# Optimization experiments

Measured on AMD Instinct MI355X. Metric: run time of the kernel, lower is better.

## Reference

```python
import jax, jax.numpy as jnp
import numpy as np

CONF = 0.25
IOU = 0.7
MAX_DET = 300
IMG_H = 1280
IMG_W = 1280
KPT_SHAPE = (17, 3)
MAX_NMS = 3000
BS = 16
N_ANCH = 33600  # (1280/8)^2 + (1280/16)^2 + (1280/32)^2


def setup_inputs() -> dict:
    key = jax.random.key(0)
    k1, k2, k3, k4 = jax.random.split(key, 4)
    # realistic YOLO head outputs: centers in image, positive w/h, conf in (0,1)
    cxy = jax.random.uniform(k1, (BS, 2, N_ANCH)) * jnp.array([IMG_W, IMG_H], jnp.float32).reshape(1, 2, 1)
    wh = jax.random.uniform(k2, (BS, 2, N_ANCH)) * 200.0 + 4.0
    conf = jax.random.uniform(k3, (BS, 1, N_ANCH))
    kpts = jax.random.uniform(k4, (BS, 51, N_ANCH)) * float(IMG_W)
    preds = jnp.concatenate([cxy, wh, conf, kpts], axis=1).astype(jnp.float32)
    return {"preds": preds}


def _pairwise_iou(boxes):
    # boxes: [M, 4] xyxy
    area = (boxes[:, 2] - boxes[:, 0]) * (boxes[:, 3] - boxes[:, 1])
    lt = jnp.maximum(boxes[:, None, :2], boxes[None, :, :2])
    rb = jnp.minimum(boxes[:, None, 2:], boxes[None, :, 2:])
    wh = jnp.clip(rb - lt, 0.0)
    inter = wh[..., 0] * wh[..., 1]
    return inter / (area[:, None] + area[None, :] - inter + 1e-9)


def _nms_keep(boxes, valid):
    # greedy NMS over score-descending boxes; returns bool keep mask [M]
    M = boxes.shape[0]
    idx = jnp.arange(M)
    supp = (_pairwise_iou(boxes) > IOU) & (idx[None, :] > idx[:, None])

    def body(i, keep):
        # row i suppresses later boxes only if it is itself kept
        return keep & ~(supp[i] & keep[i])

    return jax.lax.fori_loop(0, M, body, valid)


def _per_image(boxes_xywh, scores, kpts):
    # boxes_xywh: [N,4], scores: [N], kpts: [N,51]
    valid = scores > CONF
    masked = jnp.where(valid, scores, -1.0)
    order = jnp.argsort(-masked)[:MAX_NMS]  # top max_nms by score, desc
    b = boxes_xywh[order]
    sc = scores[order]
    kp = kpts[order]
    v = valid[order]
    # xywh -> xyxy with clip to image bounds
    cx, cy, w, h = b[:, 0], b[:, 1], b[:, 2], b[:, 3]
    x1 = jnp.clip(cx - w / 2, 0.0, IMG_W)
    y1 = jnp.clip(cy - h / 2, 0.0, IMG_H)
    x2 = jnp.clip(cx + w / 2, 0.0, IMG_W)
    y2 = jnp.clip(cy + h / 2, 0.0, IMG_H)
    bxy = jnp.stack([x1, y1, x2, y2], axis=-1)
    # faithful to original _clip_coords quirk: only channels 0 and 1 of the 51 clipped
    kp = kp.at[:, 0].set(jnp.clip(kp[:, 0], 0.0, IMG_W))
    kp = kp.at[:, 1].set(jnp.clip(kp[:, 1], 0.0, IMG_H))
    keep = _nms_keep(bxy, v)
    rank = jnp.cumsum(keep) - 1
    sel = keep & (rank < MAX_DET)
    tgt = jnp.where(sel, rank, MAX_DET)  # dropped rows scatter to slot MAX_DET (sliced off)
    ob = jnp.zeros((MAX_DET + 1, 4), bxy.dtype).at[tgt].set(jnp.where(sel[:, None], bxy, 0.0))[:MAX_DET]
    osc = jnp.zeros((MAX_DET + 1, 1), sc.dtype).at[tgt].set(jnp.where(sel[:, None], sc[:, None], 0.0))[:MAX_DET]
    okp = jnp.zeros((MAX_DET + 1, 51), kp.dtype).at[tgt].set(jnp.where(sel[:, None], kp, 0.0))[:MAX_DET]
    return ob, osc, okp


def reference(preds):
    bs = preds.shape[0]
    x = jnp.transpose(preds, (0, 2, 1))  # [bs, N, 56]
    ob, osc, okp = jax.vmap(_per_image)(x[..., :4], x[..., 4], x[..., 5:])
    return ob, osc, okp.reshape(bs, MAX_DET, *KPT_SHAPE)
```

## Files before the change

### kernel.cpp

```cpp
#include <hip/hip_runtime.h>
#include <stdint.h>

#define N_ANCH 33600
#define BS 16
#define NCH 56
#define MAX_NMS 3000
#define MAX_DET 300
#define CONF_T 0.25f
#define IOU_T 0.7f
#define IMG 1280.0f
#define NW 47
#define NBINS 4096
#define HIST_BINS 4097
#define CAP 4096
#define WCAP 4096
#define WC_STRIDE 16
#define NIT 9

#define OFF_CAND 0
#define OFF_WL   (OFF_CAND + BS*CAP*8)
#define OFF_META (OFF_WL + BS*WCAP*4)
#define OFF_BOX  ((OFF_META + BS*MAX_NMS*8 + 15) & ~15)
#define OFF_WC   (OFF_BOX + BS*MAX_NMS*16)
#define OFF_GBM  (OFF_WC + BS*WC_STRIDE*4)
#define OFF_FOI  (OFF_GBM + BS*8)

__device__ __forceinline__ int score_bucket(float c, uint32_t* bits_out) {
    if (!(c > CONF_T)) { *bits_out = 0u; return 0; }
    uint32_t bits = __float_as_uint(c);
    *bits_out = bits;
    int bucket = (int)(bits >> 12) - 0x3E800 + 1;
    bucket = bucket < 1 ? 1 : (bucket > NBINS ? NBINS : bucket);
    return bucket;
}

__device__ __forceinline__ float iou_pair(float4 bi, float ai, float4 bj) {
    float aj  = (bj.z - bj.x) * (bj.w - bj.y);
    float ltx = fmaxf(bi.x, bj.x), lty = fmaxf(bi.y, bj.y);
    float rbx = fminf(bi.z, bj.z), rby = fminf(bi.w, bj.w);
    float wx  = fmaxf(rbx - ltx, 0.f), wy = fmaxf(rby - lty, 0.f);
    float inter = wx * wy;
    return inter / (ai + aj - inter + 1e-9f);
}

__device__ __forceinline__ unsigned long long readlane64(unsigned long long v, int lane) {
    uint32_t lo = (uint32_t)v, hi = (uint32_t)(v >> 32);
    uint32_t rlo = __builtin_amdgcn_readlane(lo, lane);
    uint32_t rhi = __builtin_amdgcn_readlane(hi, lane);
    return ((unsigned long long)rhi << 32) | (unsigned long long)rlo;
}

__global__ void __launch_bounds__(1024)
k_phase1(const float* __restrict__ preds,
         unsigned long long* __restrict__ cand,
         unsigned int* __restrict__ wlist, int* __restrict__ wcount,
         int2* __restrict__ gbm) {
    __shared__ int hl[HIST_BINS];
    __shared__ int st[HIST_BINS];
    __shared__ int part[256];
    __shared__ int suf[256];
    __shared__ int ldsB, ldsM, ldsWc;
    const int b = blockIdx.x, t = threadIdx.x;
    if (t == 0) ldsWc = 0;
    for (int i = t; i < HIST_BINS; i += 1024) hl[i] = 0;
    __syncthreads();
    const float4* conf4 = (const float4*)(preds + (size_t)b * NCH * N_ANCH + 4 * N_ANCH);
    float4 rc[NIT];
    #pragma unroll
    for (int it = 0; it < NIT; it++) {
        int a4 = t + it * 1024;
        if (a4 < N_ANCH / 4) {
            float4 c4 = conf4[a4];
            rc[it] = c4;
            uint32_t bits;
            int bk;
            bk = score_bucket(c4.x, &bits); if (bk > 0) atomicAdd(&hl[bk], 1);
            bk = score_bucket(c4.y, &bits); if (bk > 0) atomicAdd(&hl[bk], 1);
            bk = score_bucket(c4.z, &bits); if (bk > 0) atomicAdd(&hl[bk], 1);
            bk = score_bucket(c4.w, &bits); if (bk > 0) atomicAdd(&hl[bk], 1);
        }
    }
    __syncthreads();
    if (t < 256) {
        int s = 0;
        for (int k = 0; k < 16; k++) s += hl[1 + t * 16 + k];
        part[t] = s;
    }
    __syncthreads();
    if (t == 0) {
        int run = 0;
        for (int i = 255; i >= 0; i--) { suf[i] = run; run += part[i]; }
        if (run < MAX_NMS) { ldsB = 1; ldsM = run; }
    }
    __syncthreads();
    if (t < 256) {
        int run = suf[t];
        bool maycross = (run < MAX_NMS) && (run + part[t] >= MAX_NMS);
        bool done = false;
        for (int k = 15; k >= 0; k--) {
            int bin = 1 + t * 16 + k;
            st[bin] = run;
            run += hl[bin];
            if (maycross && !done && run >= MAX_NMS) { ldsB = bin; ldsM = run; done = true; }
        }
    }
    __syncthreads();
    const int B = ldsB;
    if (t < 256) {
        for (int k = 0; k < 16; k++) {
            int bin = 1 + t * 16 + k;
            int c = hl[bin], s = st[bin];
            if (c > 0 && bin >= B && s < MAX_NMS) {
                int idx = atomicAdd(&ldsWc, 1);
                wlist[b * WCAP + idx] = (unsigned int)s | ((unsigned int)c << 16);
            }
        }
    }
    __syncthreads();
    #pragma unroll
    for (int it = 0; it < NIT; it++) {
        int a4 = t + it * 1024;
        if (a4 < N_ANCH / 4) {
            float4 c4 = rc[it];
            float cv[4] = {c4.x, c4.y, c4.z, c4.w};
            #pragma unroll
            for (int q = 0; q < 4; q++) {
                uint32_t bits;
                int bucket = score_bucket(cv[q], &bits);
                if (bucket >= B && bucket > 0) {
                    int pos = atomicAdd(&st[bucket], 1);
                    if (pos < CAP) {
                        int a = a4 * 4 + q;
                        cand[b * CAP + pos] =
                            ((unsigned long long)bits << 32) | (uint32_t)(~(uint32_t)a);
                    }
                }
            }
        }
    }
    if (t == 0) {
        wcount[b * WC_STRIDE] = ldsWc;
        gbm[b] = make_int2(ldsB, ldsM);
    }
}

__global__ void k_rank(const float* __restrict__ preds,
                       const unsigned long long* __restrict__ cand,
                       const unsigned int* __restrict__ wlist,
                       const int* __restrict__ wcount,
                       uint2* __restrict__ meta, float4* __restrict__ box_ws) {
    const int b = blockIdx.x;
    const int wc = wcount[b * WC_STRIDE];
    const int wv = blockIdx.y * (blockDim.x >> 6) + (threadIdx.x >> 6);
    const int lane = threadIdx.x & 63;
    const int wstride = gridDim.y * (blockDim.x >> 6);
    const float* pr = preds + (size_t)b * NCH * N_ANCH;
    for (int e = wv; e < wc; e += wstride) {
        unsigned int ent = wlist[b * WCAP + e];
        int s = (int)(ent & 0xffffu);
        int n = (int)(ent >> 16);
        if (s + n > CAP) n = CAP - s;
        const unsigned long long* seg = cand + b * CAP + s;
        for (int i = lane; i < n; i += 64) {
            unsigned long long ke = seg[i];
            int r = 0;
            for (int j = 0; j < n; j++) r += (seg[j] > ke);
            int pos = s + r;
            if (pos < MAX_NMS) {
                int oi = (int)(~(uint32_t)ke);
                uint32_t sbits = (uint32_t)(ke >> 32);
                float cx = pr[0 * N_ANCH + oi], cy = pr[1 * N_ANCH + oi];
                float w  = pr[2 * N_ANCH + oi], h  = pr[3 * N_ANCH + oi];
                float4 bx;
                bx.x = fminf(fmaxf(cx - w * 0.5f, 0.f), IMG);
                bx.y = fminf(fmaxf(cy - h * 0.5f, 0.f), IMG);
                bx.z = fminf(fmaxf(cx + w * 0.5f, 0.f), IMG);
                bx.w = fminf(fmaxf(cy + h * 0.5f, 0.f), IMG);
                box_ws[b * MAX_NMS + pos] = bx;
                meta[b * MAX_NMS + pos] = make_uint2((unsigned int)oi, sbits);
            }
        }
    }
}

__global__ void __launch_bounds__(1024)
k_nms(const float4* __restrict__ box_ws, const uint2* __restrict__ meta,
      const int2* __restrict__ gbm, int* __restrict__ foi, float* __restrict__ out) {
    __shared__ float4 lbox[MAX_NMS];
    __shared__ float4 kbox[MAX_DET];
    __shared__ float  karea[MAX_DET];
    __shared__ int    lsel[MAX_DET];
    __shared__ unsigned long long pres[NW];
    __shared__ unsigned long long diag[64];
    __shared__ unsigned long long keptmask_sh;
    const int b = blockIdx.x, t = threadIdx.x;
    const int M = gbm[b].y;
    const int Mc = M < MAX_NMS ? M : MAX_NMS;
    for (int j = t; j < Mc; j += 1024) lbox[j] = box_ws[b * MAX_NMS + j];
    if (t < NW) {
        int base = t * 64;
        int lo = Mc - base;
        unsigned long long inv = (lo <= 0) ? ~0ull : (lo >= 64 ? 0ull : ~((1ull << lo) - 1ull));
        pres[t] = inv;
    }
    __syncthreads();
    int kc = 0;
    const int nch = (Mc + 63) >> 6;
    for (int c = 0; c < nch && kc < MAX_DET; c++) {
        int base = c * 64;
        if (t < 64) diag[t] = 0ull;
        __syncthreads();
        {
            int jl = t >> 4, kk = t & 15;
            int j = base + jl;
            if (j < Mc && kc > 0) {
                float4 bj = lbox[j];
                bool sup = false;
                for (int kidx = kk; kidx < kc; kidx += 16) {
                    if (iou_pair(kbox[kidx], karea[kidx], bj) > IOU_T) { sup = true; break; }
                }
                if (sup) atomicOr(&pres[c], 1ull << jl);
            }
        }
        {
            int il = t >> 4;
            int j0 = (t & 15) * 4;
            int i = base + il;
            if (i < Mc) {
                float4 bi = lbox[i];
                float ai = (bi.z - bi.x) * (bi.w - bi.y);
                unsigned long long m = 0ull;
                for (int q = 0; q < 4; q++) {
                    int jl = j0 + q, j = base + jl;
                    if (j > i && j < Mc) {
                        if (iou_pair(bi, ai, lbox[j]) > IOU_T) m |= 1ull << jl;
                    }
                }
                if (m) atomicOr(&diag[il], m);
            }
        }
        __syncthreads();
        if (t < 64) {
            unsigned long long mydiag = diag[t];
            unsigned long long s = pres[c];
            unsigned long long keptm = 0ull;
            int room = MAX_DET - kc;
            int jmax = Mc - base; if (jmax > 64) jmax = 64;
            for (int bb = 0; bb < jmax; bb++) {
                if (!((s >> bb) & 1ull)) {
                    s |= readlane64(mydiag, bb);
                    keptm |= 1ull << bb;
                    if (--room == 0) break;
                }
            }
            if (t == 0) keptmask_sh = keptm;
        }
        __syncthreads();
        unsigned long long keptm = keptmask_sh;
        if (t < 64 && ((keptm >> t) & 1ull)) {
            int pos = kc + __popcll(keptm & ((1ull << t) - 1ull));
            float4 bx = lbox[base + t];
            kbox[pos] = bx;
            karea[pos] = (bx.z - bx.x) * (bx.w - bx.y);
            lsel[pos] = base + t;
        }
        kc += __popcll(keptm);
        __syncthreads();
    }
    float* ob  = out;
    float* osc = out + BS * MAX_DET * 4;
    for (int r = t; r < MAX_DET; r += 1024) {
        int det = b * MAX_DET + r;
        if (r < kc) {
            float4 bx = kbox[r];
            ob[det * 4 + 0] = bx.x; ob[det * 4 + 1] = bx.y;
            ob[det * 4 + 2] = bx.z; ob[det * 4 + 3] = bx.w;
            uint2 mt = meta[b * MAX_NMS + lsel[r]];
            osc[det] = __uint_as_float(mt.y);
            foi[det] = (int)mt.x;
        } else {
            ob[det * 4 + 0] = 0.f; ob[det * 4 + 1] = 0.f;
            ob[det * 4 + 2] = 0.f; ob[det * 4 + 3] = 0.f;
            osc[det] = 0.f;
            foi[det] = -1;
        }
    }
}

__global__ void k_kpt(const float* __restrict__ preds, const int* __restrict__ foi,
                      float* __restrict__ out) {
    int g = blockIdx.x * blockDim.x + threadIdx.x;
    int det = g >> 6, lane = g & 63;
    if (det >= BS * MAX_DET || lane >= 51) return;
    int b = det / MAX_DET;
    float* okp = out + BS * MAX_DET * 5;
    int oi = foi[det];
    if (oi >= 0) {
        float v = preds[(size_t)b * NCH * N_ANCH + (size_t)(5 + lane) * N_ANCH + oi];
        if (lane < 2) v = fminf(fmaxf(v, 0.f), IMG);
        okp[det * 51 + lane] = v;
    } else {
        okp[det * 51 + lane] = 0.f;
    }
}

extern "C" void kernel_launch(void* const* d_in, const int* in_sizes, int n_in,
                              void* d_out, int out_size, void* d_ws, size_t ws_size,
                              hipStream_t stream) {
    const float* preds = (const float*)d_in[0];
    float* out = (float*)d_out;
    char* ws = (char*)d_ws;
    unsigned long long* cand = (unsigned long long*)(ws + OFF_CAND);
    unsigned int* wlist = (unsigned int*)(ws + OFF_WL);
    uint2* meta = (uint2*)(ws + OFF_META);
    float4* box = (float4*)(ws + OFF_BOX);
    int* wcount = (int*)(ws + OFF_WC);
    int2* gbm = (int2*)(ws + OFF_GBM);
    int* foi = (int*)(ws + OFF_FOI);

    k_phase1<<<BS, 1024, 0, stream>>>(preds, cand, wlist, wcount, gbm);
    k_rank<<<dim3(BS, 32), 256, 0, stream>>>(preds, cand, wlist, wcount, meta, box);
    k_nms<<<BS, 1024, 0, stream>>>(box, meta, gbm, foi, out);
    k_kpt<<<(BS * MAX_DET * 64 + 255) / 256, 256, 0, stream>>>(preds, foi, out);
}
```

Before: 229.4 us.

## Fuse four NMS-stage kernels into one cooperative persistent kernel with grid syncs

Merges the histogram/candidate, ranking, NMS and keypoint-gather kernels into one cooperative launch of 256 blocks of 1024 threads, separated by grid.sync barriers. Shared memory is reused between the histogram stage and the NMS box buffer through a raw byte array. The keypoint gather becomes a dense one-thread-per-output mapping with no idle lanes. The aim is to remove per-launch overhead and inter-kernel gaps, at the cost of grid-wide barriers and a grid sized to be co-resident, which may reduce parallelism in the rank stage compared with the 512-block launch it replaces.

```diff
diff --git a/kernel.cpp b/kernel.cpp
--- a/kernel.cpp
+++ b/kernel.cpp
@@ -1,5 +1,8 @@
 #include <hip/hip_runtime.h>
+#include <hip/hip_cooperative_groups.h>
 #include <stdint.h>
+
+namespace cg = cooperative_groups;
 
 #define N_ANCH 33600
 #define BS 16
@@ -16,6 +19,7 @@
 #define WCAP 4096
 #define WC_STRIDE 16
 #define NIT 9
+#define NBLK 256
 
 #define OFF_CAND 0
 #define OFF_WL   (OFF_CAND + BS*CAP*8)
@@ -51,256 +55,260 @@
 }
 
 __global__ void __launch_bounds__(1024)
-k_phase1(const float* __restrict__ preds,
-         unsigned long long* __restrict__ cand,
-         unsigned int* __restrict__ wlist, int* __restrict__ wcount,
-         int2* __restrict__ gbm) {
-    __shared__ int hl[HIST_BINS];
-    __shared__ int st[HIST_BINS];
-    __shared__ int part[256];
-    __shared__ int suf[256];
-    __shared__ int ldsB, ldsM, ldsWc;
-    const int b = blockIdx.x, t = threadIdx.x;
-    if (t == 0) ldsWc = 0;
-    for (int i = t; i < HIST_BINS; i += 1024) hl[i] = 0;
-    __syncthreads();
-    const float4* conf4 = (const float4*)(preds + (size_t)b * NCH * N_ANCH + 4 * N_ANCH);
-    float4 rc[NIT];
-    #pragma unroll
-    for (int it = 0; it < NIT; it++) {
-        int a4 = t + it * 1024;
-        if (a4 < N_ANCH / 4) {
-            float4 c4 = conf4[a4];
-            rc[it] = c4;
-            uint32_t bits;
-            int bk;
-            bk = score_bucket(c4.x, &bits); if (bk > 0) atomicAdd(&hl[bk], 1);
-            bk = score_bucket(c4.y, &bits); if (bk > 0) atomicAdd(&hl[bk], 1);
-            bk = score_bucket(c4.z, &bits); if (bk > 0) atomicAdd(&hl[bk], 1);
-            bk = score_bucket(c4.w, &bits); if (bk > 0) atomicAdd(&hl[bk], 1);
-        }
-    }
-    __syncthreads();
-    if (t < 256) {
-        int s = 0;
-        for (int k = 0; k < 16; k++) s += hl[1 + t * 16 + k];
-        part[t] = s;
-    }
-    __syncthreads();
-    if (t == 0) {
-        int run = 0;
-        for (int i = 255; i >= 0; i--) { suf[i] = run; run += part[i]; }
-        if (run < MAX_NMS) { ldsB = 1; ldsM = run; }
-    }
-    __syncthreads();
-    if (t < 256) {
-        int run = suf[t];
-        bool maycross = (run < MAX_NMS) && (run + part[t] >= MAX_NMS);
-        bool done = false;
-        for (int k = 15; k >= 0; k--) {
-            int bin = 1 + t * 16 + k;
-            st[bin] = run;
-            run += hl[bin];
-            if (maycross && !done && run >= MAX_NMS) { ldsB = bin; ldsM = run; done = true; }
-        }
-    }
-    __syncthreads();
-    const int B = ldsB;
-    if (t < 256) {
-        for (int k = 0; k < 16; k++) {
-            int bin = 1 + t * 16 + k;
-            int c = hl[bin], s = st[bin];
-            if (c > 0 && bin >= B && s < MAX_NMS) {
-                int idx = atomicAdd(&ldsWc, 1);
-                wlist[b * WCAP + idx] = (unsigned int)s | ((unsigned int)c << 16);
-            }
-        }
-    }
-    __syncthreads();
-    #pragma unroll
-    for (int it = 0; it < NIT; it++) {
-        int a4 = t + it * 1024;
-        if (a4 < N_ANCH / 4) {
-            float4 c4 = rc[it];
-            float cv[4] = {c4.x, c4.y, c4.z, c4.w};
-            #pragma unroll
-            for (int q = 0; q < 4; q++) {
-                uint32_t bits;
-                int bucket = score_bucket(cv[q], &bits);
-                if (bucket >= B && bucket > 0) {
-                    int pos = atomicAdd(&st[bucket], 1);
-                    if (pos < CAP) {
-                        int a = a4 * 4 + q;
-                        cand[b * CAP + pos] =
-                            ((unsigned long long)bits << 32) | (uint32_t)(~(uint32_t)a);
-                    }
-                }
-            }
-        }
-    }
-    if (t == 0) {
-        wcount[b * WC_STRIDE] = ldsWc;
-        gbm[b] = make_int2(ldsB, ldsM);
-    }
-}
-
-__global__ void k_rank(const float* __restrict__ preds,
-                       const unsigned long long* __restrict__ cand,
-                       const unsigned int* __restrict__ wlist,
-                       const int* __restrict__ wcount,
-                       uint2* __restrict__ meta, float4* __restrict__ box_ws) {
-    const int b = blockIdx.x;
-    const int wc = wcount[b * WC_STRIDE];
-    const int wv = blockIdx.y * (blockDim.x >> 6) + (threadIdx.x >> 6);
-    const int lane = threadIdx.x & 63;
-    const int wstride = gridDim.y * (blockDim.x >> 6);
-    const float* pr = preds + (size_t)b * NCH * N_ANCH;
-    for (int e = wv; e < wc; e += wstride) {
-        unsigned int ent = wlist[b * WCAP + e];
-        int s = (int)(ent & 0xffffu);
-        int n = (int)(ent >> 16);
-        if (s + n > CAP) n = CAP - s;
-        const unsigned long long* seg = cand + b * CAP + s;
-        for (int i = lane; i < n; i += 64) {
-            unsigned long long ke = seg[i];
-            int r = 0;
-            for (int j = 0; j < n; j++) r += (seg[j] > ke);
-            int pos = s + r;
-            if (pos < MAX_NMS) {
-                int oi = (int)(~(uint32_t)ke);
-                uint32_t sbits = (uint32_t)(ke >> 32);
-                float cx = pr[0 * N_ANCH + oi], cy = pr[1 * N_ANCH + oi];
-                float w  = pr[2 * N_ANCH + oi], h  = pr[3 * N_ANCH + oi];
-                float4 bx;
-                bx.x = fminf(fmaxf(cx - w * 0.5f, 0.f), IMG);
-                bx.y = fminf(fmaxf(cy - h * 0.5f, 0.f), IMG);
-                bx.z = fminf(fmaxf(cx + w * 0.5f, 0.f), IMG);
-                bx.w = fminf(fmaxf(cy + h * 0.5f, 0.f), IMG);
-                box_ws[b * MAX_NMS + pos] = bx;
-                meta[b * MAX_NMS + pos] = make_uint2((unsigned int)oi, sbits);
-            }
-        }
-    }
-}
-
-__global__ void __launch_bounds__(1024)
-k_nms(const float4* __restrict__ box_ws, const uint2* __restrict__ meta,
-      const int2* __restrict__ gbm, int* __restrict__ foi, float* __restrict__ out) {
-    __shared__ float4 lbox[MAX_NMS];
+k_mega(const float* __restrict__ preds,
+       unsigned long long* __restrict__ cand,
+       unsigned int* __restrict__ wlist, int* __restrict__ wcount,
+       int2* __restrict__ gbm,
+       uint2* __restrict__ meta, float4* __restrict__ box_ws,
+       int* __restrict__ foi, float* __restrict__ out) {
+    cg::grid_group grid = cg::this_grid();
+    __shared__ __align__(16) char sraw[48000];
     __shared__ float4 kbox[MAX_DET];
     __shared__ float  karea[MAX_DET];
     __shared__ int    lsel[MAX_DET];
     __shared__ unsigned long long pres[NW];
     __shared__ unsigned long long diag[64];
     __shared__ unsigned long long keptmask_sh;
-    const int b = blockIdx.x, t = threadIdx.x;
-    const int M = gbm[b].y;
-    const int Mc = M < MAX_NMS ? M : MAX_NMS;
-    for (int j = t; j < Mc; j += 1024) lbox[j] = box_ws[b * MAX_NMS + j];
-    if (t < NW) {
-        int base = t * 64;
-        int lo = Mc - base;
-        unsigned long long inv = (lo <= 0) ? ~0ull : (lo >= 64 ? 0ull : ~((1ull << lo) - 1ull));
-        pres[t] = inv;
+    __shared__ int ldsB, ldsM, ldsWc;
+    const int blk = blockIdx.x, t = threadIdx.x;
+
+    if (blk < BS) {
+        const int b = blk;
+        int* hl   = (int*)sraw;
+        int* st   = (int*)(sraw + 16388);
+        int* part = (int*)(sraw + 32776);
+        int* suf  = (int*)(sraw + 33800);
+        if (t == 0) ldsWc = 0;
+        for (int i = t; i < HIST_BINS; i += 1024) hl[i] = 0;
+        __syncthreads();
+        const float4* conf4 = (const float4*)(preds + (size_t)b * NCH * N_ANCH + 4 * N_ANCH);
+        float4 rc[NIT];
+        #pragma unroll
+        for (int it = 0; it < NIT; it++) {
+            int a4 = t + it * 1024;
+            if (a4 < N_ANCH / 4) {
+                float4 c4 = conf4[a4];
+                rc[it] = c4;
+                uint32_t bits;
+                int bk;
+                bk = score_bucket(c4.x, &bits); if (bk > 0) atomicAdd(&hl[bk], 1);
+                bk = score_bucket(c4.y, &bits); if (bk > 0) atomicAdd(&hl[bk], 1);
+                bk = score_bucket(c4.z, &bits); if (bk > 0) atomicAdd(&hl[bk], 1);
+                bk = score_bucket(c4.w, &bits); if (bk > 0) atomicAdd(&hl[bk], 1);
+            }
+        }
+        __syncthreads();
+        if (t < 256) {
+            int s = 0;
+            for (int k = 0; k < 16; k++) s += hl[1 + t * 16 + k];
+            part[t] = s;
+        }
+        __syncthreads();
+        if (t == 0) {
+            int run = 0;
+            for (int i = 255; i >= 0; i--) { suf[i] = run; run += part[i]; }
+            if (run < MAX_NMS) { ldsB = 1; ldsM = run; }
+        }
+        __syncthreads();
+        if (t < 256) {
+            int run = suf[t];
+            bool maycross = (run < MAX_NMS) && (run + part[t] >= MAX_NMS);
+            bool done = false;
+            for (int k = 15; k >= 0; k--) {
+                int bin = 1 + t * 16 + k;
+                st[bin] = run;
+                run += hl[bin];
+                if (maycross && !done && run >= MAX_NMS) { ldsB = bin; ldsM = run; done = true; }
+            }
+        }
+        __syncthreads();
+        const int B = ldsB;
+        if (t < 256) {
+            for (int k = 0; k < 16; k++) {
+                int bin = 1 + t * 16 + k;
+                int c = hl[bin], s = st[bin];
+                if (c > 0 && bin >= B && s < MAX_NMS) {
+                    int idx = atomicAdd(&ldsWc, 1);
+                    wlist[b * WCAP + idx] = (unsigned int)s | ((unsigned int)c << 16);
+                }
+            }
+        }
+        __syncthreads();
+        #pragma unroll
+        for (int it = 0; it < NIT; it++) {
+            int a4 = t + it * 1024;
+            if (a4 < N_ANCH / 4) {
+                float4 c4 = rc[it];
+                float cv[4] = {c4.x, c4.y, c4.z, c4.w};
+                #pragma unroll
+                for (int q = 0; q < 4; q++) {
+                    uint32_t bits;
+                    int bucket = score_bucket(cv[q], &bits);
+                    if (bucket >= B && bucket > 0) {
+                        int pos = atomicAdd(&st[bucket], 1);
+                        if (pos < CAP) {
+                            int a = a4 * 4 + q;
+                            cand[b * CAP + pos] =
+                                ((unsigned long long)bits << 32) | (uint32_t)(~(uint32_t)a);
+                        }
+                    }
+                }
+            }
+        }
+        if (t == 0) {
+            wcount[b * WC_STRIDE] = ldsWc;
+            gbm[b] = make_int2(ldsB, ldsM);
+        }
     }
-    __syncthreads();
-    int kc = 0;
-    const int nch = (Mc + 63) >> 6;
-    for (int c = 0; c < nch && kc < MAX_DET; c++) {
-        int base = c * 64;
-        if (t < 64) diag[t] = 0ull;
-        __syncthreads();
-        {
-            int jl = t >> 4, kk = t & 15;
-            int j = base + jl;
-            if (j < Mc && kc > 0) {
-                float4 bj = lbox[j];
-                bool sup = false;
-                for (int kidx = kk; kidx < kc; kidx += 16) {
-                    if (iou_pair(kbox[kidx], karea[kidx], bj) > IOU_T) { sup = true; break; }
-                }
-                if (sup) atomicOr(&pres[c], 1ull << jl);
-            }
-        }
-        {
-            int il = t >> 4;
-            int j0 = (t & 15) * 4;
-            int i = base + il;
-            if (i < Mc) {
-                float4 bi = lbox[i];
-                float ai = (bi.z - bi.x) * (bi.w - bi.y);
-                unsigned long long m = 0ull;
-                for (int q = 0; q < 4; q++) {
-                    int jl = j0 + q, j = base + jl;
-                    if (j > i && j < Mc) {
-                        if (iou_pair(bi, ai, lbox[j]) > IOU_T) m |= 1ull << jl;
+    grid.sync();
+
+    {
+        const int gw = blk * 16 + (t >> 6);
+        const int lane = t & 63;
+        const int b = gw & 15;
+        const int wv = gw >> 4;
+        const int wc = wcount[b * WC_STRIDE];
+        const float* pr = preds + (size_t)b * NCH * N_ANCH;
+        for (int e = wv; e < wc; e += 256) {
+            unsigned int ent = wlist[b * WCAP + e];
+            int s = (int)(ent & 0xffffu);
+            int n = (int)(ent >> 16);
+            if (s + n > CAP) n = CAP - s;
+            const unsigned long long* seg = cand + b * CAP + s;
+            for (int i = lane; i < n; i += 64) {
+                unsigned long long ke = seg[i];
+                int r = 0;
+                for (int j = 0; j < n; j++) r += (seg[j] > ke);
+                int pos = s + r;
+                if (pos < MAX_NMS) {
+                    int oi = (int)(~(uint32_t)ke);
+                    uint32_t sbits = (uint32_t)(ke >> 32);
+                    float cx = pr[0 * N_ANCH + oi], cy = pr[1 * N_ANCH + oi];
+                    float w  = pr[2 * N_ANCH + oi], h  = pr[3 * N_ANCH + oi];
+                    float4 bx;
+                    bx.x = fminf(fmaxf(cx - w * 0.5f, 0.f), IMG);
+                    bx.y = fminf(fmaxf(cy - h * 0.5f, 0.f), IMG);
+                    bx.z = fminf(fmaxf(cx + w * 0.5f, 0.f), IMG);
+                    bx.w = fminf(fmaxf(cy + h * 0.5f, 0.f), IMG);
+                    box_ws[b * MAX_NMS + pos] = bx;
+                    meta[b * MAX_NMS + pos] = make_uint2((unsigned int)oi, sbits);
+                }
+            }
+        }
+    }
+    grid.sync();
+
+    if (blk < BS) {
+        const int b = blk;
+        float4* lbox = (float4*)sraw;
+        const int M = gbm[b].y;
+        const int Mc = M < MAX_NMS ? M : MAX_NMS;
+        for (int j = t; j < Mc; j += 1024) lbox[j] = box_ws[b * MAX_NMS + j];
+        if (t < NW) {
+            int base = t * 64;
+            int lo = Mc - base;
+            unsigned long long inv = (lo <= 0) ? ~0ull : (lo >= 64 ? 0ull : ~((1ull << lo) - 1ull));
+            pres[t] = inv;
+        }
+        __syncthreads();
+        int kc = 0;
+        const int nch = (Mc + 63) >> 6;
+        for (int c = 0; c < nch && kc < MAX_DET; c++) {
+            int base = c * 64;
+            if (t < 64) diag[t] = 0ull;
+            __syncthreads();
+            {
+                int jl = t >> 4, kk = t & 15;
+                int j = base + jl;
+                if (j < Mc && kc > 0) {
+                    float4 bj = lbox[j];
+                    bool sup = false;
+                    for (int kidx = kk; kidx < kc; kidx += 16) {
+                        if (iou_pair(kbox[kidx], karea[kidx], bj) > IOU_T) { sup = true; break; }
                     }
-                }
-                if (m) atomicOr(&diag[il], m);
-            }
-        }
-        __syncthreads();
-        if (t < 64) {
-            unsigned long long mydiag = diag[t];
-            unsigned long long s = pres[c];
-            unsigned long long keptm = 0ull;
-            int room = MAX_DET - kc;
-            int jmax = Mc - base; if (jmax > 64) jmax = 64;
-            for (int bb = 0; bb < jmax; bb++) {
-                if (!((s >> bb) & 1ull)) {
-                    s |= readlane64(mydiag, bb);
-                    keptm |= 1ull << bb;
-                    if (--room == 0) break;
-                }
-            }
-            if (t == 0) keptmask_sh = keptm;
-        }
-        __syncthreads();
-        unsigned long long keptm = keptmask_sh;
-        if (t < 64 && ((keptm >> t) & 1ull)) {
-            int pos = kc + __popcll(keptm & ((1ull << t) - 1ull));
-            float4 bx = lbox[base + t];
-            kbox[pos] = bx;
-            karea[pos] = (bx.z - bx.x) * (bx.w - bx.y);
-            lsel[pos] = base + t;
-        }
-        kc += __popcll(keptm);
-        __syncthreads();
+                    if (sup) atomicOr(&pres[c], 1ull << jl);
+                }
+            }
+            {
+                int il = t >> 4;
+                int j0 = (t & 15) * 4;
+                int i = base + il;
+                if (i < Mc) {
+                    float4 bi = lbox[i];
+                    float ai = (bi.z - bi.x) * (bi.w - bi.y);
+                    unsigned long long m = 0ull;
+                    for (int q = 0; q < 4; q++) {
+                        int jl = j0 + q, j = base + jl;
+                        if (j > i && j < Mc) {
+                            if (iou_pair(bi, ai, lbox[j]) > IOU_T) m |= 1ull << jl;
+                        }
+                    }
+                    if (m) atomicOr(&diag[il], m);
+                }
+            }
+            __syncthreads();
+            if (t < 64) {
+                unsigned long long mydiag = diag[t];
+                unsigned long long s = pres[c];
+                unsigned long long keptm = 0ull;
+                int room = MAX_DET - kc;
+                int jmax = Mc - base; if (jmax > 64) jmax = 64;
+                for (int bb = 0; bb < jmax; bb++) {
+                    if (!((s >> bb) & 1ull)) {
+                        s |= readlane64(mydiag, bb);
+                        keptm |= 1ull << bb;
+                        if (--room == 0) break;
+                    }
+                }
+                if (t == 0) keptmask_sh = keptm;
+            }
+            __syncthreads();
+            unsigned long long keptm = keptmask_sh;
+            if (t < 64 && ((keptm >> t) & 1ull)) {
+                int pos = kc + __popcll(keptm & ((1ull << t) - 1ull));
+                float4 bx = lbox[base + t];
+                kbox[pos] = bx;
+                karea[pos] = (bx.z - bx.x) * (bx.w - bx.y);
+                lsel[pos] = base + t;
+            }
+            kc += __popcll(keptm);
+            __syncthreads();
+        }
+        float* ob  = out;
+        float* osc = out + BS * MAX_DET * 4;
+        for (int r = t; r < MAX_DET; r += 1024) {
+            int det = b * MAX_DET + r;
+            if (r < kc) {
+                float4 bx = kbox[r];
+                ob[det * 4 + 0] = bx.x; ob[det * 4 + 1] = bx.y;
+                ob[det * 4 + 2] = bx.z; ob[det * 4 + 3] = bx.w;
+                uint2 mt = meta[b * MAX_NMS + lsel[r]];
+                osc[det] = __uint_as_float(mt.y);
+                foi[det] = (int)mt.x;
+            } else {
+                ob[det * 4 + 0] = 0.f; ob[det * 4 + 1] = 0.f;
+                ob[det * 4 + 2] = 0.f; ob[det * 4 + 3] = 0.f;
+                osc[det] = 0.f;
+                foi[det] = -1;
+            }
+        }
     }
-    float* ob  = out;
-    float* osc = out + BS * MAX_DET * 4;
-    for (int r = t; r < MAX_DET; r += 1024) {
-        int det = b * MAX_DET + r;
-        if (r < kc) {
-            float4 bx = kbox[r];
-            ob[det * 4 + 0] = bx.x; ob[det * 4 + 1] = bx.y;
-            ob[det * 4 + 2] = bx.z; ob[det * 4 + 3] = bx.w;
-            uint2 mt = meta[b * MAX_NMS + lsel[r]];
-            osc[det] = __uint_as_float(mt.y);
-            foi[det] = (int)mt.x;
-        } else {
-            ob[det * 4 + 0] = 0.f; ob[det * 4 + 1] = 0.f;
-            ob[det * 4 + 2] = 0.f; ob[det * 4 + 3] = 0.f;
-            osc[det] = 0.f;
-            foi[det] = -1;
-        }
-    }
-}
-
-__global__ void k_kpt(const float* __restrict__ preds, const int* __restrict__ foi,
-                      float* __restrict__ out) {
-    int g = blockIdx.x * blockDim.x + threadIdx.x;
-    int det = g >> 6, lane = g & 63;
-    if (det >= BS * MAX_DET || lane >= 51) return;
-    int b = det / MAX_DET;
-    float* okp = out + BS * MAX_DET * 5;
-    int oi = foi[det];
-    if (oi >= 0) {
-        float v = preds[(size_t)b * NCH * N_ANCH + (size_t)(5 + lane) * N_ANCH + oi];
-        if (lane < 2) v = fminf(fmaxf(v, 0.f), IMG);
-        okp[det * 51 + lane] = v;
-    } else {
-        okp[det * 51 + lane] = 0.f;
+    grid.sync();
+
+    {
+        const int g = blk * 1024 + t;
+        if (g < BS * MAX_DET * 51) {
+            int det = g / 51, lane = g - det * 51;
+            int b = det / MAX_DET;
+            float* okp = out + BS * MAX_DET * 5;
+            int oi = foi[det];
+            float v = 0.f;
+            if (oi >= 0) {
+                v = preds[(size_t)b * NCH * N_ANCH + (size_t)(5 + lane) * N_ANCH + oi];
+                if (lane < 2) v = fminf(fmaxf(v, 0.f), IMG);
+            }
+            okp[g] = v;
+        }
     }
 }
 
@@ -318,8 +326,8 @@
     int2* gbm = (int2*)(ws + OFF_GBM);
     int* foi = (int*)(ws + OFF_FOI);
 
-    k_phase1<<<BS, 1024, 0, stream>>>(preds, cand, wlist, wcount, gbm);
-    k_rank<<<dim3(BS, 32), 256, 0, stream>>>(preds, cand, wlist, wcount, meta, box);
-    k_nms<<<BS, 1024, 0, stream>>>(box, meta, gbm, foi, out);
-    k_kpt<<<(BS * MAX_DET * 64 + 255) / 256, 256, 0, stream>>>(preds, foi, out);
-}
+    void* args[] = {(void*)&preds, (void*)&cand, (void*)&wlist, (void*)&wcount,
+                    (void*)&gbm, (void*)&meta, (void*)&box, (void*)&foi, (void*)&out};
+    hipLaunchCooperativeKernel((const void*)k_mega, dim3(NBLK), dim3(1024),
+                               args, 0, stream);
+}
```

Result: slower. 308.8 us (+34.6%).
